# Kernel tuning notes

Measured on AMD Instinct MI355X. Metric: run time of the kernel, lower is better.

The kernel has to match this reference:

```python
import jax, jax.numpy as jnp
import numpy as np
import math

TRACKS = 512       # tracks_number == number of rows of x (module implicitly assumes this)
FEATURES = 256
# torch code does torch.tensor(1e-46).log(); we use the intended finite value log(1e-46).
# (In strict fp32 torch, 1e-46 underflows to 0 and log gives -inf, which poisons grads with NaN;
#  we use the mathematically intended finite constant, cast to fp32.)
MASK_VAL = np.float32(math.log(1e-46))  # ~ -105.9189


def setup_inputs() -> dict:
    key = jax.random.key(0)
    kx, kw, kb = jax.random.split(key, 3)
    x = jax.random.normal(kx, (TRACKS, FEATURES), dtype=jnp.float32)
    # nn.Linear(features_number, 1) parameters
    W = jax.random.normal(kw, (1, FEATURES), dtype=jnp.float32) / math.sqrt(FEATURES)
    b = jax.random.normal(kb, (1,), dtype=jnp.float32) / math.sqrt(FEATURES)
    return {"x": x, "W": W, "b": b}


def reference(x, W, b):
    # scores: (tracks, 1)
    scores = x @ W.T + b
    # argmax over the flattened (tracks, 1) tensor == row argmax
    idx = jnp.argmax(scores)
    # delete_row: mask of ones with log(1e-46) at argmax position
    mask = jnp.ones((TRACKS,), dtype=jnp.float32).at[idx].set(MASK_VAL)
    # mm(scores (T,1), mask (1,T)) -> outer product block (T, T)
    block = scores * mask[None, :]
    # the torch loop never updates `scores`, so all tracks_number concatenated
    # blocks are identical -> tile instead of a Python loop of concats
    rep = jnp.tile(block, (1, TRACKS))  # tracks_number == TRACKS repetitions
    return jnp.concatenate([scores, rep], axis=1)  # (T, 1 + T*T)
```

## Files before the change

### kernel.cpp

```cpp
#include <hip/hip_runtime.h>
#include <hip/hip_bf16.h>


#define TRACKS 512
#define FEATURES 256
#define ROWSTRIDE 262145LL
#define BULK 262144
#define MASK_VAL (-105.918914f)

#define BPR 16
#define CHUNK (BULK / BPR)

typedef float vf4 __attribute__((ext_vector_type(4)));

__global__ __launch_bounds__(64) void scores_kernel(
    const float* __restrict__ x, const float* __restrict__ W,
    const float* __restrict__ b, float* __restrict__ scores) {
  int row = blockIdx.x;
  int lane = threadIdx.x;
  const float4* xr = (const float4*)(x + row * FEATURES);
  const float4* wr = (const float4*)W;
  float4 xv = xr[lane];
  float4 wv = wr[lane];
  float s = xv.x * wv.x + xv.y * wv.y + xv.z * wv.z + xv.w * wv.w;
#pragma unroll
  for (int off = 32; off; off >>= 1) s += __shfl_down(s, off);
  if (lane == 0) scores[row] = s + b[0];
}

__global__ __launch_bounds__(512) void argmax_kernel(
    const float* __restrict__ scores, int* __restrict__ idx_out,
    float* __restrict__ out) {
  __shared__ float svals[TRACKS];
  __shared__ int sidx[TRACKS];
  int t = threadIdx.x;
  float v = scores[t];
  out[(long long)t * ROWSTRIDE] = v;
  svals[t] = v;
  sidx[t] = t;
  __syncthreads();
  for (int off = 256; off; off >>= 1) {
    if (t < off) {
      float v2 = svals[t + off];
      int i2 = sidx[t + off];
      if (v2 > svals[t] || (v2 == svals[t] && i2 < sidx[t])) {
        svals[t] = v2;
        sidx[t] = i2;
      }
    }
    __syncthreads();
  }
  if (t == 0) idx_out[0] = sidx[0];
}

__global__ __launch_bounds__(256) void fill_kernel(
    const float* __restrict__ scores, const int* __restrict__ idxp,
    float* __restrict__ out) {
  int row = blockIdx.x / BPR;
  int blk = blockIdx.x % BPR;
  int t = threadIdx.x;

  float s = scores[row];
  int idx = *idxp;
  float sm = s * MASK_VAL;

  long long S = (long long)row * ROWSTRIDE + 1;
  long long lo = S + (long long)blk * CHUNK;

  int align = (int)((4 - (lo & 3)) & 3);
  if (t < align) {
    long long p = lo + t;
    int j = (int)((p - S) & 511);
    out[p] = (j == idx) ? sm : s;
  }

  int nrem = CHUNK - align;
  int nf4 = nrem >> 2;
  int tail = nrem & 3;
  long long abase = lo + align;

  int j0 = (int)((abase - S + 4 * t) & 511);
  vf4 val;
  val.x = (j0 == idx) ? sm : s;
  val.y = (((j0 + 1) & 511) == idx) ? sm : s;
  val.z = (((j0 + 2) & 511) == idx) ? sm : s;
  val.w = (((j0 + 3) & 511) == idx) ? sm : s;

  vf4* outv = (vf4*)(out + abase);
  for (int k = t; k < nf4; k += 256) {
    outv[k] = val;
  }

  if (t < tail) {
    long long p = abase + 4LL * nf4 + t;
    int j = (int)((p - S) & 511);
    out[p] = (j == idx) ? sm : s;
  }
}

extern "C" void kernel_launch(void* const* d_in, const int* in_sizes, int n_in,
                              void* d_out, int out_size, void* d_ws,
                              size_t ws_size, hipStream_t stream) {
  const float* x = (const float*)d_in[0];
  const float* W = (const float*)d_in[1];
  const float* b = (const float*)d_in[2];
  float* out = (float*)d_out;

  float* scores = (float*)d_ws;
  int* idx = (int*)((float*)d_ws + TRACKS);

  scores_kernel<<<TRACKS, 64, 0, stream>>>(x, W, b, scores);
  argmax_kernel<<<1, TRACKS, 0, stream>>>(scores, idx, out);
  fill_kernel<<<TRACKS * BPR, 256, 0, stream>>>(scores, idx, out);
}
```

Measured before the change: 536.7 us.

## Fill output as one flat aligned float4 stream with grid-stride loop

Replaces the per-row chunked fill, which needed scalar head and tail stores for misaligned row starts, with a flat grid-stride kernel that treats the entire output as aligned float4 stores. Each thread works out the row and column from the flat index, so the first-column score values are written inside the same stream and the argmax kernel no longer writes them. This aims for fully coalesced, uniform vector stores, at the cost of extra index arithmetic and per-element scores loads.

```diff
diff --git a/kernel.cpp b/kernel.cpp
--- a/kernel.cpp
+++ b/kernel.cpp
@@ -1,15 +1,14 @@
 #include <hip/hip_runtime.h>
-#include <hip/hip_bf16.h>
 
 
 #define TRACKS 512
 #define FEATURES 256
-#define ROWSTRIDE 262145LL
-#define BULK 262144
+#define ROWSTRIDE 262145
 #define MASK_VAL (-105.918914f)
 
-#define BPR 16
-#define CHUNK (BULK / BPR)
+#define TOTAL_F4 33554560u
+#define FILL_BLOCKS 32768
+#define FILL_TPB 256
 
 typedef float vf4 __attribute__((ext_vector_type(4)));
 
@@ -29,13 +28,11 @@
 }
 
 __global__ __launch_bounds__(512) void argmax_kernel(
-    const float* __restrict__ scores, int* __restrict__ idx_out,
-    float* __restrict__ out) {
+    const float* __restrict__ scores, int* __restrict__ idx_out) {
   __shared__ float svals[TRACKS];
   __shared__ int sidx[TRACKS];
   int t = threadIdx.x;
   float v = scores[t];
-  out[(long long)t * ROWSTRIDE] = v;
   svals[t] = v;
   sidx[t] = t;
   __syncthreads();
@@ -53,48 +50,44 @@
   if (t == 0) idx_out[0] = sidx[0];
 }
 
-__global__ __launch_bounds__(256) void fill_kernel(
+__global__ __launch_bounds__(FILL_TPB) void fill_flat(
     const float* __restrict__ scores, const int* __restrict__ idxp,
     float* __restrict__ out) {
-  int row = blockIdx.x / BPR;
-  int blk = blockIdx.x % BPR;
-  int t = threadIdx.x;
-
-  float s = scores[row];
+  unsigned g = blockIdx.x * FILL_TPB + threadIdx.x;
   int idx = *idxp;
-  float sm = s * MASK_VAL;
-
-  long long S = (long long)row * ROWSTRIDE + 1;
-  long long lo = S + (long long)blk * CHUNK;
-
-  int align = (int)((4 - (lo & 3)) & 3);
-  if (t < align) {
-    long long p = lo + t;
-    int j = (int)((p - S) & 511);
-    out[p] = (j == idx) ? sm : s;
-  }
-
-  int nrem = CHUNK - align;
-  int nf4 = nrem >> 2;
-  int tail = nrem & 3;
-  long long abase = lo + align;
-
-  int j0 = (int)((abase - S + 4 * t) & 511);
-  vf4 val;
-  val.x = (j0 == idx) ? sm : s;
-  val.y = (((j0 + 1) & 511) == idx) ? sm : s;
-  val.z = (((j0 + 2) & 511) == idx) ? sm : s;
-  val.w = (((j0 + 3) & 511) == idx) ? sm : s;
-
-  vf4* outv = (vf4*)(out + abase);
-  for (int k = t; k < nf4; k += 256) {
-    outv[k] = val;
-  }
-
-  if (t < tail) {
-    long long p = abase + 4LL * nf4 + t;
-    int j = (int)((p - S) & 511);
-    out[p] = (j == idx) ? sm : s;
+  vf4* outv = (vf4*)out;
+  for (; g < TOTAL_F4; g += (unsigned)FILL_BLOCKS * FILL_TPB) {
+    unsigned p = g << 2;
+    unsigned q = p >> 18;
+    int rem = (int)p - (int)((q << 18) + q);
+    int row = (int)q;
+    if (rem < 0) { row -= 1; rem += ROWSTRIDE; }
+    float s = scores[row];
+    float sm = s * MASK_VAL;
+    vf4 val;
+    {
+      float v = (((rem - 1) & 511) == idx) ? sm : s;
+      val.x = (rem == 0) ? s : v;
+    }
+    rem++;
+    if (rem == ROWSTRIDE) { rem = 0; row++; s = scores[row]; sm = s * MASK_VAL; }
+    {
+      float v = (((rem - 1) & 511) == idx) ? sm : s;
+      val.y = (rem == 0) ? s : v;
+    }
+    rem++;
+    if (rem == ROWSTRIDE) { rem = 0; row++; s = scores[row]; sm = s * MASK_VAL; }
+    {
+      float v = (((rem - 1) & 511) == idx) ? sm : s;
+      val.z = (rem == 0) ? s : v;
+    }
+    rem++;
+    if (rem == ROWSTRIDE) { rem = 0; row++; s = scores[row]; sm = s * MASK_VAL; }
+    {
+      float v = (((rem - 1) & 511) == idx) ? sm : s;
+      val.w = (rem == 0) ? s : v;
+    }
+    outv[g] = val;
   }
 }
 
@@ -110,6 +103,6 @@
   int* idx = (int*)((float*)d_ws + TRACKS);
 
   scores_kernel<<<TRACKS, 64, 0, stream>>>(x, W, b, scores);
-  argmax_kernel<<<1, TRACKS, 0, stream>>>(scores, idx, out);
-  fill_kernel<<<TRACKS * BPR, 256, 0, stream>>>(scores, idx, out);
+  argmax_kernel<<<1, TRACKS, 0, stream>>>(scores, idx);
+  fill_flat<<<FILL_BLOCKS, FILL_TPB, 0, stream>>>(scores, idx, out);
 }
```

After: 512.9 us (median of 2 runs). 1.05x faster.
